# Performance work log

Measured on AMD Instinct MI355X. Metric: run time of the kernel, lower is better.

The kernel has to match this reference:

```python
import jax, jax.numpy as jnp
import numpy as np

G = 3  # group_num
EPS = 1e-5


def _ln(x, g, b):
    m = x.mean(-1, keepdims=True)
    v = x.var(-1, keepdims=True)
    return (x - m) / jnp.sqrt(v + EPS) * g + b


def _gcm(x, w_qk, b_qk, ct_w1, ct_b1, ct_g, ct_be, ct_w2, ct_b2,
         lw_w1, lw_b1, lw_g, lw_be, lw_w2, lw_b2):
    # x: [B, 768, H, W] (pre-concatenated group feature)
    b, c, h, w = x.shape
    gc = c // G
    # channel shuffle: b (g c) h w -> b (c g) h w
    xs = x.reshape(b, G, gc, h, w).transpose(0, 2, 1, 3, 4).reshape(b, c, h, w)
    out = xs.reshape(b, G, gc, h, w)            # b g c h w
    value = out.reshape(b, G, gc, h * w)        # b g c n
    # fc_qk (Linear gc->1) over the channel axis, softmax over spatial n
    logits = jnp.einsum('bgcn,c->bgn', value, w_qk) + b_qk
    attn = jax.nn.softmax(logits, axis=-1)       # b g n
    context = jnp.einsum('bgcn,bgn->bgc', value, attn)  # b g c
    lvl_context = context.reshape(b, c)          # b (g c)
    # ctx_transform: Linear -> LN -> ReLU -> Linear
    h1 = jax.nn.relu(_ln(context @ ct_w1.T + ct_b1, ct_g, ct_be))
    ctx = h1 @ ct_w2.T + ct_b2                   # b g c
    # lvl_weight: Linear -> LN -> ReLU -> Linear -> Sigmoid
    l1 = jax.nn.relu(_ln(lvl_context @ lw_w1.T + lw_b1, lw_g, lw_be))
    lvlw = jax.nn.sigmoid(l1 @ lw_w2.T + lw_b2)  # b g (=3)
    ctx = ctx * lvlw[:, :, None]
    return (out + ctx[:, :, :, None, None]).sum(axis=1)  # b c_g h w


def setup_inputs() -> dict:
    key = jax.random.key(0)
    ks = jax.random.split(key, 16)
    B = 8
    sizes = [(128, 128), (64, 64), (32, 32), (16, 16)]
    inp = {}
    for i, (h, w) in enumerate(sizes):
        inp[f'g{i}'] = jax.random.normal(ks[i], (B, 768, h, w), jnp.float32)
    inp['x_last'] = jax.random.normal(ks[4], (B, 256, 8, 8), jnp.float32)
    s = 0.05
    inp['w_qk'] = jax.random.normal(ks[5], (4, 256), jnp.float32) * s
    inp['b_qk'] = jax.random.normal(ks[6], (4,), jnp.float32) * s
    inp['ct_w1'] = jax.random.normal(ks[7], (4, 64, 256), jnp.float32) * s
    inp['ct_b1'] = jax.random.normal(ks[8], (4, 64), jnp.float32) * s
    inp['ct_g'] = jnp.ones((4, 64), jnp.float32)
    inp['ct_be'] = jnp.zeros((4, 64), jnp.float32)
    inp['ct_w2'] = jax.random.normal(ks[9], (4, 256, 64), jnp.float32) * s
    inp['ct_b2'] = jax.random.normal(ks[10], (4, 256), jnp.float32) * s
    inp['lw_w1'] = jax.random.normal(ks[11], (4, 768, 768), jnp.float32) * s
    inp['lw_b1'] = jax.random.normal(ks[12], (4, 768), jnp.float32) * s
    inp['lw_g'] = jnp.ones((4, 768), jnp.float32)
    inp['lw_be'] = jnp.zeros((4, 768), jnp.float32)
    inp['lw_w2'] = jax.random.normal(ks[13], (4, 3, 768), jnp.float32) * s
    inp['lw_b2'] = jax.random.normal(ks[14], (4, 3), jnp.float32) * s
    return inp


def reference(g0, g1, g2, g3, x_last, w_qk, b_qk, ct_w1, ct_b1, ct_g, ct_be,
              ct_w2, ct_b2, lw_w1, lw_b1, lw_g, lw_be, lw_w2, lw_b2):
    outs = []
    for i, g in enumerate([g0, g1, g2, g3]):
        outs.append(_gcm(g, w_qk[i], b_qk[i], ct_w1[i], ct_b1[i], ct_g[i],
                         ct_be[i], ct_w2[i], ct_b2[i], lw_w1[i], lw_b1[i],
                         lw_g[i], lw_be[i], lw_w2[i], lw_b2[i]))
    return (*outs, x_last)
```

## Files before the change

kernel.cpp:

```cpp
#include <hip/hip_runtime.h>

#define NB 8
#define T 32
#define TPW 8
#define NWG 680
#define PSTRIDE 772

typedef float f4 __attribute__((ext_vector_type(4)));

__device__ __forceinline__ f4 ntload(const float* p) {
  return __builtin_nontemporal_load((const f4*)p);
}
__device__ __forceinline__ void ntstore(float* p, f4 v) {
  __builtin_nontemporal_store(v, (f4*)p);
}
__device__ __forceinline__ float hsum(f4 v) { return v.x + v.y + v.z + v.w; }

struct KFArgs {
  const float* x[4];
  float* outp[4];
  float* partial;
  int N[4];
};

__global__ __launch_bounds__(512) void kf_fused(KFArgs a, const float* __restrict__ wqk_all) {
  extern __shared__ float lds[];
  float* xt   = lds;
  float* swq  = xt + 768 * T;
  float* red  = swq + 256;
  float* se   = red + 768;
  float* zred = se + 96;

  int wg = blockIdx.x;
  int lvl, b, t0;
  if (wg < 512)      { lvl = 0; b = wg >> 6;        t0 = (wg & 63) * TPW; }
  else if (wg < 640) { int r = wg - 512; lvl = 1; b = r >> 4; t0 = (r & 15) * TPW; }
  else if (wg < 672) { int r = wg - 640; lvl = 2; b = r >> 2; t0 = (r & 3) * TPW; }
  else               { int r = wg - 672; lvl = 3; b = r;      t0 = 0; }
  int N = a.N[lvl];
  const float* __restrict__ xb = a.x[lvl] + (size_t)b * 768 * N;
  float* __restrict__ outb = a.outp[lvl] + (size_t)b * 256 * N;
  int tid = threadIdx.x;

  if (tid < 256) swq[tid] = wqk_all[lvl * 256 + tid];

  float accA = 0.f, accB = 0.f;
  float zacc = 0.f;

  int snq = tid & 7, srow0 = tid >> 3;
  f4 reg[12];
  {
    int n0 = t0 * T;
#pragma unroll
    for (int i = 0; i < 12; ++i) {
      int s = srow0 + i * 64;
      reg[i] = ntload(xb + (size_t)s * N + n0 + snq * 4);
    }
  }

  for (int tt = 0; tt < TPW; ++tt) {
    int n0 = (t0 + tt) * T;
    __syncthreads();
#pragma unroll
    for (int i = 0; i < 12; ++i) {
      int s = srow0 + i * 64;
      int f = (s & 255) * 3 + (s >> 8);
      *(f4*)(xt + f * T + snq * 4) = reg[i];
    }
    __syncthreads();
    if (tid < 256) {
      int n = tid & 31, cb = tid >> 5;
      float l0 = 0.f, l1 = 0.f, l2 = 0.f;
      const float* w = swq + cb * 32;
      const float* base = xt + (cb * 32) * T + n;
#pragma unroll 8
      for (int c = 0; c < 32; ++c) {
        float wv = w[c];
        l0 = fmaf(base[c * T], wv, l0);
        l1 = fmaf(base[(256 + c) * T], wv, l1);
        l2 = fmaf(base[(512 + c) * T], wv, l2);
      }
      red[cb * 96 + 0 * 32 + n] = l0;
      red[cb * 96 + 1 * 32 + n] = l1;
      red[cb * 96 + 2 * 32 + n] = l2;
    } else {
      int t2 = tid - 256;
#pragma unroll
      for (int k = 0; k < 8; ++k) {
        int item = t2 + k * 256;
        int c2 = item >> 3, nq = item & 7;
        const float* p = xt + c2 * T + nq * 4;
        f4 v = *(const f4*)p + *(const f4*)(p + 256 * T) + *(const f4*)(p + 512 * T);
        *(f4*)(outb + (size_t)c2 * N + n0 + nq * 4) = v;
      }
    }
    __syncthreads();
    if (tid < 96) {
      int g = tid >> 5, n = tid & 31;
      float l = 0.f;
#pragma unroll
      for (int cb = 0; cb < 8; ++cb) l += red[cb * 96 + g * 32 + n];
      float e = __expf(l);
      se[g * 32 + n] = e;
      zacc += e;
    }
    __syncthreads();
    if (tt + 1 < TPW) {
      int n0n = (t0 + tt + 1) * T;
#pragma unroll
      for (int i = 0; i < 12; ++i) {
        int s = srow0 + i * 64;
        reg[i] = ntload(xb + (size_t)s * N + n0n + snq * 4);
      }
    }
    {
      int lane = tid & 63;
      int g = tid >> 8;
      const float* xr = xt + tid * T;
      const float* er = se + g * 32;
      float acc = 0.f;
#pragma unroll 8
      for (int i = 0; i < 32; ++i) {
        int nn = (i + lane) & 31;
        acc = fmaf(xr[nn], er[nn], acc);
      }
      accA += acc;
      if (tid < 256) {
        const float* xr2 = xt + (tid + 512) * T;
        const float* er2 = se + 64;
        float acc2 = 0.f;
#pragma unroll 8
        for (int i = 0; i < 32; ++i) {
          int nn = (i + lane) & 31;
          acc2 = fmaf(xr2[nn], er2[nn], acc2);
        }
        accB += acc2;
      }
    }
  }
  float* pw = a.partial + (size_t)wg * PSTRIDE;
  pw[tid] = accA;
  if (tid < 256) pw[tid + 512] = accB;
  if (tid < 96) zred[tid] = zacc;
  __syncthreads();
  if (tid < 3) {
    float z = 0.f;
#pragma unroll
    for (int i = 0; i < 32; ++i) z += zred[tid * 32 + i];
    pw[768 + tid] = z;
  }
}

__device__ __forceinline__ float blk_sum256(float v, float* sr4) {
  for (int o = 32; o; o >>= 1) v += __shfl_xor(v, o);
  __syncthreads();
  if ((threadIdx.x & 63) == 0) sr4[threadIdx.x >> 6] = v;
  __syncthreads();
  return sr4[0] + sr4[1] + sr4[2] + sr4[3];
}

__global__ __launch_bounds__(256) void k4_mlp(
    const float* __restrict__ partial,
    const float* __restrict__ ct_w1, const float* __restrict__ ct_b1,
    const float* __restrict__ ct_g,  const float* __restrict__ ct_be,
    const float* __restrict__ ct_w2, const float* __restrict__ ct_b2,
    const float* __restrict__ lw_w1, const float* __restrict__ lw_b1,
    const float* __restrict__ lw_g,  const float* __restrict__ lw_be,
    const float* __restrict__ lw_w2, const float* __restrict__ lw_b2,
    float* __restrict__ add_all) {
  int b = blockIdx.x, lvl = blockIdx.y;
  int t = threadIdx.x;
  static const int cnt_[4] = {64, 16, 4, 1};
  static const int base_[4] = {0, 512, 640, 672};
  int cnt = cnt_[lvl];
  int wg0 = base_[lvl] + b * cnt;

  const float* w1 = ct_w1 + lvl * 64 * 256;
  const float* b1 = ct_b1 + lvl * 64;
  const float* cg = ct_g + lvl * 64;
  const float* cbe = ct_be + lvl * 64;
  const float* w2 = ct_w2 + lvl * 256 * 64;
  const float* b2 = ct_b2 + lvl * 256;
  const float* W1 = lw_w1 + (size_t)lvl * 768 * 768;
  const float* B1 = lw_b1 + lvl * 768;
  const float* Lg = lw_g + lvl * 768;
  const float* Lbe = lw_be + lvl * 768;
  const float* W2 = lw_w2 + lvl * 3 * 768;
  const float* B2 = lw_b2 + lvl * 3;
  float* addp = add_all + ((size_t)lvl * NB + b) * 256;

  __shared__ float sctx[768];
  __shared__ float sh1[3][64];
  __shared__ float sl1[768];
  __shared__ float slvlw[3];
  __shared__ float sr4[4];
  __shared__ float sZ[3];

  float s0 = 0.f, s1 = 0.f, s2 = 0.f;
  for (int w = 0; w < cnt; ++w) {
    const float* pw = partial + (size_t)(wg0 + w) * PSTRIDE;
    s0 += pw[t];
    s1 += pw[t + 256];
    s2 += pw[t + 512];
  }
  if (t < 3) {
    float z = 0.f;
    for (int w = 0; w < cnt; ++w) z += partial[(size_t)(wg0 + w) * PSTRIDE + 768 + t];
    sZ[t] = z;
  }
  __syncthreads();
  sctx[t] = s0 / sZ[0];
  sctx[t + 256] = s1 / sZ[1];
  sctx[t + 512] = s2 / sZ[2];
  __syncthreads();

  if (t < 192) {
    int g = t >> 6, j = t & 63;
    const f4* w4 = (const f4*)(w1 + j * 256);
    const f4* c4 = (const f4*)(sctx + g * 256);
    f4 acc = {0.f, 0.f, 0.f, 0.f};
#pragma unroll 8
    for (int k = 0; k < 64; ++k) acc += c4[k] * w4[k];
    sh1[g][j] = hsum(acc) + b1[j];
  }
  __syncthreads();
  int wv = t >> 6, ln = t & 63;
  if (wv < 3) {
    float v = sh1[wv][ln];
    float s = v;
    for (int o = 32; o; o >>= 1) s += __shfl_xor(s, o);
    float mean = s * (1.f / 64.f);
    float d = v - mean;
    float q = d * d;
    for (int o = 32; o; o >>= 1) q += __shfl_xor(q, o);
    float var = q * (1.f / 64.f);
    float y = d * rsqrtf(var + 1e-5f) * cg[ln] + cbe[ln];
    sh1[wv][ln] = fmaxf(y, 0.f);
  }
  __syncthreads();
  float l1v[3];
#pragma unroll
  for (int r = 0; r < 3; ++r) {
    int j = t + r * 256;
    const f4* W4 = (const f4*)(W1 + (size_t)j * 768);
    const f4* s4 = (const f4*)sctx;
    f4 acc = {0.f, 0.f, 0.f, 0.f};
#pragma unroll 8
    for (int k = 0; k < 192; ++k) acc += s4[k] * W4[k];
    l1v[r] = hsum(acc) + B1[j];
  }
  float S = blk_sum256(l1v[0] + l1v[1] + l1v[2], sr4);
  float mean = S * (1.f / 768.f);
  float q = 0.f;
#pragma unroll
  for (int r = 0; r < 3; ++r) { float d = l1v[r] - mean; q += d * d; }
  float var = blk_sum256(q, sr4) * (1.f / 768.f);
  float inv = rsqrtf(var + 1e-5f);
#pragma unroll
  for (int r = 0; r < 3; ++r) {
    int j = t + r * 256;
    float y = (l1v[r] - mean) * inv * Lg[j] + Lbe[j];
    sl1[j] = fmaxf(y, 0.f);
  }
  __syncthreads();
  if (wv < 3) {
    float acc = 0.f;
    for (int j = ln; j < 768; j += 64) acc = fmaf(sl1[j], W2[wv * 768 + j], acc);
    for (int o = 32; o; o >>= 1) acc += __shfl_xor(acc, o);
    if (ln == 0) slvlw[wv] = 1.f / (1.f + __expf(-(acc + B2[wv])));
  }
  __syncthreads();
  {
    int c2 = t;
    float a = 0.f;
#pragma unroll
    for (int g = 0; g < 3; ++g) {
      const f4* w4 = (const f4*)(w2 + c2 * 64);
      const f4* h4 = (const f4*)(sh1[g]);
      f4 acc = {0.f, 0.f, 0.f, 0.f};
#pragma unroll
      for (int j = 0; j < 16; ++j) acc += h4[j] * w4[j];
      a += (hsum(acc) + b2[c2]) * slvlw[g];
    }
    addp[c2] = a;
  }
}

__global__ __launch_bounds__(256) void k5_add(float* __restrict__ out,
                                              const float* __restrict__ add_all,
                                              const float* __restrict__ xlast) {
  size_t f4i = (size_t)blockIdx.x * 256 + threadIdx.x;
  if (f4i >= 11141120) {
    size_t r = f4i - 11141120;
    f4 v = ntload(xlast + (r << 2));
    ntstore(out + (f4i << 2), v);
    return;
  }
  int lvl, lgN2;
  size_t base;
  if (f4i < 8388608)       { lvl = 0; base = 0;        lgN2 = 12; }
  else if (f4i < 10485760) { lvl = 1; base = 8388608;  lgN2 = 10; }
  else if (f4i < 11010048) { lvl = 2; base = 10485760; lgN2 = 8;  }
  else                     { lvl = 3; base = 11010048; lgN2 = 6;  }
  size_t lf4 = f4i - base;
  int bc = (int)(lf4 >> lgN2);
  float a = add_all[lvl * 2048 + bc];
  float* p = out + (f4i << 2);
  f4 v = *(const f4*)p;
  v += a;
  ntstore(p, v);
}

extern "C" void kernel_launch(void* const* d_in, const int* in_sizes, int n_in,
                              void* d_out, int out_size, void* d_ws, size_t ws_size,
                              hipStream_t stream) {
  const float* gx[4] = {(const float*)d_in[0], (const float*)d_in[1],
                        (const float*)d_in[2], (const float*)d_in[3]};
  const float* x_last = (const float*)d_in[4];
  const float* w_qk = (const float*)d_in[5];
  const float* ct_w1 = (const float*)d_in[7];
  const float* ct_b1 = (const float*)d_in[8];
  const float* ct_g  = (const float*)d_in[9];
  const float* ct_be = (const float*)d_in[10];
  const float* ct_w2 = (const float*)d_in[11];
  const float* ct_b2 = (const float*)d_in[12];
  const float* lw_w1 = (const float*)d_in[13];
  const float* lw_b1 = (const float*)d_in[14];
  const float* lw_g  = (const float*)d_in[15];
  const float* lw_be = (const float*)d_in[16];
  const float* lw_w2 = (const float*)d_in[17];
  const float* lw_b2 = (const float*)d_in[18];
  float* out = (float*)d_out;
  float* ws = (float*)d_ws;

  static const int Ns[4] = {16384, 4096, 1024, 256};
  static const size_t outOff[4] = {0, 33554432, 41943040, 44040192};

  float* partb = ws;
  float* addb  = ws + NWG * PSTRIDE;

  KFArgs af;
  for (int i = 0; i < 4; ++i) {
    af.x[i] = gx[i];
    af.outp[i] = out + outOff[i];
    af.N[i] = Ns[i];
  }
  af.partial = partb;

  const int ldsBytes = (768 * T + 256 + 768 + 96 + 96) * 4;
  static int attrSet = 0;
  if (!attrSet) {
    (void)hipFuncSetAttribute((const void*)kf_fused,
                              hipFuncAttributeMaxDynamicSharedMemorySize, ldsBytes);
    attrSet = 1;
  }

  kf_fused<<<dim3(NWG), dim3(512), ldsBytes, stream>>>(af, w_qk);
  k4_mlp<<<dim3(NB, 4), dim3(256), 0, stream>>>(partb, ct_w1, ct_b1, ct_g, ct_be,
                                                ct_w2, ct_b2, lw_w1, lw_b1, lw_g,
                                                lw_be, lw_w2, lw_b2, addb);
  k5_add<<<dim3(43648), dim3(256), 0, stream>>>(out, addb, x_last);
}
```

Before: 298.7 us.

## Halve spatial tile, pad LDS rows, and accumulate context from registers

The fused pooling kernel now processes 16-column tiles (16 tiles per workgroup) instead of 32, with LDS rows padded to 20 floats to avoid bank conflicts, and launch bounds request 4 workgroups per CU. The context accumulation now reads the staged register tiles directly instead of re-reading transposed rows from LDS, followed by a final LDS reduction of per-thread partials. Double-buffered register prefetch is issued right after the LDS store, earlier than before. This cuts LDS footprint and traffic to raise occupancy and overlap loads, at the cost of more tile iterations and barriers per workgroup.

```diff
diff --git a/kernel.cpp b/kernel.cpp
--- a/kernel.cpp
+++ b/kernel.cpp
@@ -1,10 +1,11 @@
 #include <hip/hip_runtime.h>
 
 #define NB 8
-#define T 32
-#define TPW 8
+#define T 16
+#define TPW 16
 #define NWG 680
 #define PSTRIDE 772
+#define XP 20
 
 typedef float f4 __attribute__((ext_vector_type(4)));
 
@@ -15,6 +16,7 @@
   __builtin_nontemporal_store(v, (f4*)p);
 }
 __device__ __forceinline__ float hsum(f4 v) { return v.x + v.y + v.z + v.w; }
+__device__ __forceinline__ int fmap(int s) { return (s & 255) * 3 + (s >> 8); }
 
 struct KFArgs {
   const float* x[4];
@@ -23,130 +25,128 @@
   int N[4];
 };
 
-__global__ __launch_bounds__(512) void kf_fused(KFArgs a, const float* __restrict__ wqk_all) {
+__global__ __launch_bounds__(512, 4) void kf_fused(KFArgs a, const float* __restrict__ wqk_all) {
   extern __shared__ float lds[];
   float* xt   = lds;
-  float* swq  = xt + 768 * T;
+  float* swq  = xt + 768 * XP;
   float* red  = swq + 256;
   float* se   = red + 768;
-  float* zred = se + 96;
+  float* zred = se + 48;
 
   int wg = blockIdx.x;
-  int lvl, b, t0;
-  if (wg < 512)      { lvl = 0; b = wg >> 6;        t0 = (wg & 63) * TPW; }
-  else if (wg < 640) { int r = wg - 512; lvl = 1; b = r >> 4; t0 = (r & 15) * TPW; }
-  else if (wg < 672) { int r = wg - 640; lvl = 2; b = r >> 2; t0 = (r & 3) * TPW; }
-  else               { int r = wg - 672; lvl = 3; b = r;      t0 = 0; }
+  int lvl, b, idx;
+  if (wg < 512)      { lvl = 0; b = wg >> 6;            idx = wg & 63; }
+  else if (wg < 640) { int r = wg - 512; lvl = 1; b = r >> 4; idx = r & 15; }
+  else if (wg < 672) { int r = wg - 640; lvl = 2; b = r >> 2; idx = r & 3; }
+  else               { int r = wg - 672; lvl = 3; b = r;      idx = 0; }
   int N = a.N[lvl];
+  int col0 = idx * 256;
   const float* __restrict__ xb = a.x[lvl] + (size_t)b * 768 * N;
   float* __restrict__ outb = a.outp[lvl] + (size_t)b * 256 * N;
   int tid = threadIdx.x;
+  int snq = tid & 3, srow0 = tid >> 2;
 
   if (tid < 256) swq[tid] = wqk_all[lvl * 256 + tid];
 
-  float accA = 0.f, accB = 0.f;
+  float acc[6] = {0.f, 0.f, 0.f, 0.f, 0.f, 0.f};
   float zacc = 0.f;
 
-  int snq = tid & 7, srow0 = tid >> 3;
-  f4 reg[12];
+  f4 regA[6], regB[6];
   {
-    int n0 = t0 * T;
-#pragma unroll
-    for (int i = 0; i < 12; ++i) {
-      int s = srow0 + i * 64;
-      reg[i] = ntload(xb + (size_t)s * N + n0 + snq * 4);
-    }
-  }
-
-  for (int tt = 0; tt < TPW; ++tt) {
-    int n0 = (t0 + tt) * T;
+    int n0 = col0;
+#pragma unroll
+    for (int i = 0; i < 6; ++i) {
+      int s = srow0 + (i << 7);
+      regA[i] = ntload(xb + (size_t)s * N + n0 + snq * 4);
+    }
+  }
+
+  auto body = [&](f4* cur, f4* nxt, int tt, bool pre) {
+    int n0 = col0 + tt * T;
+#pragma unroll
+    for (int i = 0; i < 6; ++i) {
+      int s = srow0 + (i << 7);
+      int f = fmap(s);
+      *(f4*)(xt + f * XP + snq * 4) = cur[i];
+    }
     __syncthreads();
-#pragma unroll
-    for (int i = 0; i < 12; ++i) {
-      int s = srow0 + i * 64;
-      int f = (s & 255) * 3 + (s >> 8);
-      *(f4*)(xt + f * T + snq * 4) = reg[i];
-    }
-    __syncthreads();
+    if (pre) {
+      int n0n = n0 + T;
+#pragma unroll
+      for (int i = 0; i < 6; ++i) {
+        int s = srow0 + (i << 7);
+        nxt[i] = ntload(xb + (size_t)s * N + n0n + snq * 4);
+      }
+    }
     if (tid < 256) {
-      int n = tid & 31, cb = tid >> 5;
+      int n = tid & 15, cb = tid >> 4;
       float l0 = 0.f, l1 = 0.f, l2 = 0.f;
-      const float* w = swq + cb * 32;
-      const float* base = xt + (cb * 32) * T + n;
-#pragma unroll 8
-      for (int c = 0; c < 32; ++c) {
+      const float* base = xt + (cb * 16) * XP + n;
+      const float* w = swq + cb * 16;
+#pragma unroll
+      for (int c = 0; c < 16; ++c) {
         float wv = w[c];
-        l0 = fmaf(base[c * T], wv, l0);
-        l1 = fmaf(base[(256 + c) * T], wv, l1);
-        l2 = fmaf(base[(512 + c) * T], wv, l2);
+        l0 = fmaf(base[c * XP], wv, l0);
+        l1 = fmaf(base[(256) * XP + c * XP], wv, l1);
+        l2 = fmaf(base[(512) * XP + c * XP], wv, l2);
       }
-      red[cb * 96 + 0 * 32 + n] = l0;
-      red[cb * 96 + 1 * 32 + n] = l1;
-      red[cb * 96 + 2 * 32 + n] = l2;
+      red[cb * 48 + 0 * 16 + n] = l0;
+      red[cb * 48 + 1 * 16 + n] = l1;
+      red[cb * 48 + 2 * 16 + n] = l2;
     } else {
       int t2 = tid - 256;
 #pragma unroll
-      for (int k = 0; k < 8; ++k) {
-        int item = t2 + k * 256;
-        int c2 = item >> 3, nq = item & 7;
-        const float* p = xt + c2 * T + nq * 4;
-        f4 v = *(const f4*)p + *(const f4*)(p + 256 * T) + *(const f4*)(p + 512 * T);
+      for (int k = 0; k < 4; ++k) {
+        int item = t2 + (k << 8);
+        int c2 = item >> 2, nq = item & 3;
+        const float* p = xt + c2 * XP + nq * 4;
+        f4 v = *(const f4*)p + *(const f4*)(p + 256 * XP) + *(const f4*)(p + 512 * XP);
         *(f4*)(outb + (size_t)c2 * N + n0 + nq * 4) = v;
       }
     }
     __syncthreads();
-    if (tid < 96) {
-      int g = tid >> 5, n = tid & 31;
+    if (tid < 48) {
+      int g = tid >> 4, n = tid & 15;
       float l = 0.f;
 #pragma unroll
-      for (int cb = 0; cb < 8; ++cb) l += red[cb * 96 + g * 32 + n];
+      for (int cb = 0; cb < 16; ++cb) l += red[cb * 48 + g * 16 + n];
       float e = __expf(l);
-      se[g * 32 + n] = e;
+      se[g * 16 + n] = e;
       zacc += e;
     }
     __syncthreads();
-    if (tt + 1 < TPW) {
-      int n0n = (t0 + tt + 1) * T;
-#pragma unroll
-      for (int i = 0; i < 12; ++i) {
-        int s = srow0 + i * 64;
-        reg[i] = ntload(xb + (size_t)s * N + n0n + snq * 4);
-      }
-    }
-    {
-      int lane = tid & 63;
-      int g = tid >> 8;
-      const float* xr = xt + tid * T;
-      const float* er = se + g * 32;
-      float acc = 0.f;
-#pragma unroll 8
-      for (int i = 0; i < 32; ++i) {
-        int nn = (i + lane) & 31;
-        acc = fmaf(xr[nn], er[nn], acc);
-      }
-      accA += acc;
-      if (tid < 256) {
-        const float* xr2 = xt + (tid + 512) * T;
-        const float* er2 = se + 64;
-        float acc2 = 0.f;
-#pragma unroll 8
-        for (int i = 0; i < 32; ++i) {
-          int nn = (i + lane) & 31;
-          acc2 = fmaf(xr2[nn], er2[nn], acc2);
-        }
-        accB += acc2;
-      }
-    }
-  }
+#pragma unroll
+    for (int i = 0; i < 6; ++i) {
+      int s = srow0 + (i << 7);
+      int g = fmap(s) >> 8;
+      const float* ep = se + g * 16 + snq * 4;
+      f4 v = cur[i];
+      acc[i] = fmaf(v.x, ep[0], acc[i]);
+      acc[i] = fmaf(v.y, ep[1], acc[i]);
+      acc[i] = fmaf(v.z, ep[2], acc[i]);
+      acc[i] = fmaf(v.w, ep[3], acc[i]);
+    }
+  };
+
+  for (int tt = 0; tt < TPW; tt += 2) {
+    body(regA, regB, tt, true);
+    body(regB, regA, tt + 1, tt + 1 < TPW - 1);
+  }
+
+#pragma unroll
+  for (int i = 0; i < 6; ++i) {
+    int s = srow0 + (i << 7);
+    xt[fmap(s) * 4 + snq] = acc[i];
+  }
+  if (tid < 48) zred[tid] = zacc;
+  __syncthreads();
   float* pw = a.partial + (size_t)wg * PSTRIDE;
-  pw[tid] = accA;
-  if (tid < 256) pw[tid + 512] = accB;
-  if (tid < 96) zred[tid] = zacc;
-  __syncthreads();
+  for (int r = tid; r < 768; r += 512)
+    pw[r] = xt[r * 4] + xt[r * 4 + 1] + xt[r * 4 + 2] + xt[r * 4 + 3];
   if (tid < 3) {
     float z = 0.f;
 #pragma unroll
-    for (int i = 0; i < 32; ++i) z += zred[tid * 32 + i];
+    for (int i = 0; i < 16; ++i) z += zred[tid * 16 + i];
     pw[768 + tid] = z;
   }
 }
@@ -347,7 +347,7 @@
   }
   af.partial = partb;
 
-  const int ldsBytes = (768 * T + 256 + 768 + 96 + 96) * 4;
+  const int ldsBytes = (768 * XP + 256 + 768 + 48 + 48) * 4;
   static int attrSet = 0;
   if (!attrSet) {
     (void)hipFuncSetAttribute((const void*)kf_fused,
```

After: 596.7 us. +99.8%, slower.
